# Kernel tuning notes

Hardware: AMD Instinct MI355X
Metric: run time of the kernel (lower is better)

## Reference

```python
import jax, jax.numpy as jnp
import numpy as np

SR = 44100
D = SR * 30          # duration_samples = 1_323_000
N = 1024             # number of note events
L = 32768            # max note length in samples
W = 1024             # hann window length (module's window_length)
H = 8                # harmonics in the synth
K = 128              # FIR taps in the effect chain
LAT = 2              # time_latent_size


def setup_inputs() -> dict:
    key = jax.random.key(0)
    ks = jax.random.split(key, 10)
    freq_rad = jax.random.uniform(ks[0], (N,), jnp.float32, 0.01, 0.3)
    velocity = jax.random.uniform(ks[1], (N,), jnp.float32, 1.0, 127.0)
    starts = jax.random.randint(ks[2], (N,), 0, D - L, dtype=jnp.int32)
    lengths = jax.random.randint(ks[3], (N,), 2048, L + 1, dtype=jnp.int32)
    # time_embedder: Linear(1,32) -> ReLU -> Linear(32,LAT)
    w1 = jax.random.normal(ks[4], (1, 32), jnp.float32)
    b1 = jnp.zeros((32,), jnp.float32)
    w2 = jax.random.normal(ks[5], (32, LAT), jnp.float32) / jnp.sqrt(32.0)
    b2 = jnp.zeros((LAT,), jnp.float32)
    # synth amplitude MLP: [freq, vel, latent] (2+LAT) -> 64 -> H
    ws1 = jax.random.normal(ks[6], (2 + LAT, 64), jnp.float32)
    bs1 = jnp.zeros((64,), jnp.float32)
    ws2 = jax.random.normal(ks[7], (64, H), jnp.float32) / 8.0
    bs2 = jnp.zeros((H,), jnp.float32)
    # effect chain: causal FIR (OIW layout) + tanh
    fir = jax.random.normal(ks[8], (1, 1, K), jnp.float32) / K
    return dict(freq_rad=freq_rad, velocity=velocity,
                w1=w1, b1=b1, w2=w2, b2=b2,
                ws1=ws1, bs1=bs1, ws2=ws2, bs2=bs2, fir=fir,
                starts=starts, lengths=lengths, duration_samples=D)


def reference(freq_rad, velocity, w1, b1, w2, b2, ws1, bs1, ws2, bs2, fir,
              starts, lengths, duration_samples):
    Dn = int(duration_samples)
    t = jnp.arange(L, dtype=jnp.float32)            # [L]
    ti = jnp.arange(L, dtype=jnp.int32)             # [L]
    ends = starts + lengths
    # output_length = min(end, duration) - start, clipped to [0, L]
    out_len = jnp.clip(jnp.minimum(ends, Dn) - starts, 0, L)  # [N]
    # time latent: MLP on normalized start time
    nt = (starts.astype(jnp.float32) / Dn)[:, None]           # [N,1]
    lat = jax.nn.relu(nt @ w1 + b1) @ w2 + b2                  # [N,LAT]
    vel = (velocity / 127.0)[:, None]                          # [N,1]
    # harmonic amplitudes from tiny MLP (the 'synth')
    feat = jnp.concatenate([freq_rad[:, None], vel, lat], axis=-1)  # [N,2+LAT]
    amps = jax.nn.softplus(jax.nn.relu(feat @ ws1 + bs1) @ ws2 + bs2)  # [N,H]
    # additive synthesis; fixed small loop over harmonics, vectorized over [N,L]
    phase = freq_rad[:, None] * t[None, :]                     # [N,L]
    seg = jnp.zeros((N, L), jnp.float32)
    for hh in range(1, H + 1):
        seg = seg + amps[:, hh - 1:hh] * jnp.sin(hh * phase)
    seg = seg * vel
    # hann window (torch periodic) on the LAST W samples of each variable-length segment
    n = jnp.arange(W, dtype=jnp.float32)
    hann = 0.5 * (1.0 - jnp.cos(2.0 * jnp.pi * n / W))         # [W]
    wpos = ti[None, :] - (out_len[:, None] - W)                # [N,L]
    in_win = (wpos >= 0) & (wpos < W)
    factor = jnp.where(in_win, hann[jnp.clip(wpos, 0, W - 1)], 1.0)
    mask = (ti[None, :] < out_len[:, None]).astype(jnp.float32)  # zero past segment end
    seg = seg * factor * mask
    # effect chain: causal 128-tap FIR then tanh (masked so padding stays silent)
    y = jax.lax.conv_general_dilated(seg[:, None, :], fir,
                                     window_strides=(1,), padding=[(K - 1, 0)])
    seg = jnp.tanh(y[:, 0, :]) * mask                          # [N,L]
    # overlap-add: scatter each note into the output buffer
    idx = starts[:, None] + ti[None, :]                        # [N,L]
    valid = (ti[None, :] < out_len[:, None]) & (idx < Dn)
    contrib = jnp.where(valid, seg, 0.0)
    out = jnp.zeros((Dn,), jnp.float32).at[jnp.clip(idx, 0, Dn - 1).reshape(-1)].add(
        contrib.reshape(-1))
    return out
```

## Files before the change

kernel.cpp:

```cpp
#include <hip/hip_runtime.h>
#include <math.h>

#define LMAX  32768
#define WWIN  1024
#define KFIR  128
#define WOUT  512
#define TO    1024
#define CPAD  656
#define NMAX  1024
#define PMAX  96

typedef _Float16 v8h __attribute__((ext_vector_type(8)));
typedef _Float16 v4h __attribute__((ext_vector_type(4)));
typedef float    v4f __attribute__((ext_vector_type(4)));

__device__ __forceinline__ float fast_tanh(float x) {
    float e = __builtin_amdgcn_exp2f(x * 2.8853900817779268f);
    return fmaf(-2.0f, __builtin_amdgcn_rcpf(e + 1.0f), 1.0f);
}

__global__ __launch_bounds__(128, 3) void synth_fused_k(
    const float* __restrict__ freq_g, const float* __restrict__ velo_g,
    const float* __restrict__ w1,  const float* __restrict__ b1,
    const float* __restrict__ w2,  const float* __restrict__ b2,
    const float* __restrict__ ws1, const float* __restrict__ bs1,
    const float* __restrict__ ws2, const float* __restrict__ bs2,
    const float* __restrict__ fir,
    const int* __restrict__ starts, const int* __restrict__ lengths,
    float* __restrict__ out, int Dn, int N)
{
    __shared__ __align__(16) _Float16 segc[2][4][CPAD];
    __shared__ float fir_s[KFIR];
    __shared__ unsigned short note_list[NMAX];
    __shared__ int note_cnt;
    __shared__ float s_w1[32], s_b1[32], s_w2[64], s_b2[2];
    __shared__ float s_ws1[256], s_bs1[64], s_ws2[512], s_bs2[8];
    __shared__ int   stl[PMAX], oll[PMAX];
    __shared__ float fl[PMAX];
    __shared__ __align__(16) float ampsl[PMAX][8];

    const int tid  = threadIdx.x;
    const int wid  = tid >> 6;
    const int lane = tid & 63;
    const int m    = lane & 15;
    const int quad = lane >> 4;
    const int o0   = blockIdx.x * TO;
    const int o_end = min(o0 + TO, Dn);
    const int ow   = o0 + wid * WOUT;

    fir_s[tid] = fir[tid];
    if (tid < 32) { s_w1[tid] = w1[tid]; s_b1[tid] = b1[tid]; }
    if (tid < 64) { s_w2[tid] = w2[tid]; s_bs1[tid] = bs1[tid]; }
    if (tid < 2)  s_b2[tid] = b2[tid];
    if (tid < 8)  s_bs2[tid] = bs2[tid];
    s_ws1[tid] = ws1[tid];       s_ws1[tid + 128] = ws1[tid + 128];
    s_ws2[tid] = ws2[tid];       s_ws2[tid + 128] = ws2[tid + 128];
    s_ws2[tid + 256] = ws2[tid + 256]; s_ws2[tid + 384] = ws2[tid + 384];
    if (tid == 0) note_cnt = 0;
    __syncthreads();

    for (int j = tid; j < N; j += 128) {
        int st = starts[j];
        int len = lengths[j];
        int ol = min(st + len, Dn) - st;
        ol = max(0, min(ol, LMAX));
        if (st < o_end && st + ol > o0) {
            int p = atomicAdd(&note_cnt, 1);
            note_list[p] = (unsigned short)j;
        }
    }
    __syncthreads();
    const int K = note_cnt;

    const int kn0 = min(K, PMAX);
    if (tid < kn0) {
        const int nid = (int)note_list[tid];
        int st  = starts[nid];
        int len = lengths[nid];
        int ol  = min(st + len, Dn) - st;
        ol = max(0, min(ol, LMAX));
        stl[tid] = st;
        oll[tid] = ol;
        float v = velo_g[nid] * (1.0f / 127.0f);
        float f = freq_g[nid];
        fl[tid] = f;
        float nt = (float)st / (float)Dn;
        float lat0 = s_b2[0], lat1 = s_b2[1];
        #pragma unroll
        for (int j = 0; j < 32; ++j) {
            float h = fmaxf(fmaf(nt, s_w1[j], s_b1[j]), 0.0f);
            lat0 = fmaf(h, s_w2[j * 2 + 0], lat0);
            lat1 = fmaf(h, s_w2[j * 2 + 1], lat1);
        }
        float acc[8];
        #pragma unroll
        for (int h = 0; h < 8; ++h) acc[h] = s_bs2[h];
        #pragma unroll
        for (int j = 0; j < 64; ++j) {
            float a = s_bs1[j];
            a = fmaf(f,    s_ws1[0 * 64 + j], a);
            a = fmaf(v,    s_ws1[1 * 64 + j], a);
            a = fmaf(lat0, s_ws1[2 * 64 + j], a);
            a = fmaf(lat1, s_ws1[3 * 64 + j], a);
            a = fmaxf(a, 0.0f);
            #pragma unroll
            for (int h = 0; h < 8; ++h)
                acc[h] = fmaf(a, s_ws2[j * 8 + h], acc[h]);
        }
        #pragma unroll
        for (int h = 0; h < 8; ++h) {
            float a = acc[h];
            float sp = fmaxf(a, 0.0f) + log1pf(expf(-fabsf(a)));
            ampsl[tid][h] = sp * v;
        }
    }

    v8h afrag[12];
    #pragma unroll
    for (int t = 0; t < 12; ++t) {
        v8h af;
        #pragma unroll
        for (int j = 0; j < 8; ++j) {
            int idx = 32 * t + 8 * quad + j - 16 * m;
            float fv = (idx >= 0 && idx < KFIR) ? fir_s[idx] : 0.0f;
            af[j] = (_Float16)fv;
        }
        afrag[t] = af;
    }
    for (int z = lane; z < 4 * 20; z += 64) {
        int S = z / 20, off = z % 20;
        segc[wid][S][636 + off] = (_Float16)0.0f;
    }
    __syncthreads();

    const _Float16* __restrict__ bbase = &segc[wid][m & 3][(m & ~3) + 8 * quad];

    float accA0 = 0.f, accA1 = 0.f, accA2 = 0.f, accA3 = 0.f;
    float accB0 = 0.f, accB1 = 0.f, accB2 = 0.f, accB3 = 0.f;

    const double inv2pi = 0.15915494309189535;

    for (int c = 0; c < K; c += PMAX) {
        const int kn = min(K - c, PMAX);

        if (c > 0) {
            __syncthreads();
            if (tid < kn) {
                const int nid = (int)note_list[c + tid];
                int st  = starts[nid];
                int len = lengths[nid];
                int ol  = min(st + len, Dn) - st;
                ol = max(0, min(ol, LMAX));
                stl[tid] = st;
                oll[tid] = ol;
                float v = velo_g[nid] * (1.0f / 127.0f);
                float f = freq_g[nid];
                fl[tid] = f;
                float nt = (float)st / (float)Dn;
                float lat0 = s_b2[0], lat1 = s_b2[1];
                #pragma unroll
                for (int j = 0; j < 32; ++j) {
                    float h = fmaxf(fmaf(nt, s_w1[j], s_b1[j]), 0.0f);
                    lat0 = fmaf(h, s_w2[j * 2 + 0], lat0);
                    lat1 = fmaf(h, s_w2[j * 2 + 1], lat1);
                }
                float acc[8];
                #pragma unroll
                for (int h = 0; h < 8; ++h) acc[h] = s_bs2[h];
                #pragma unroll
                for (int j = 0; j < 64; ++j) {
                    float a = s_bs1[j];
                    a = fmaf(f,    s_ws1[0 * 64 + j], a);
                    a = fmaf(v,    s_ws1[1 * 64 + j], a);
                    a = fmaf(lat0, s_ws1[2 * 64 + j], a);
                    a = fmaf(lat1, s_ws1[3 * 64 + j], a);
                    a = fmaxf(a, 0.0f);
                    #pragma unroll
                    for (int h = 0; h < 8; ++h)
                        acc[h] = fmaf(a, s_ws2[j * 8 + h], acc[h]);
                }
                #pragma unroll
                for (int h = 0; h < 8; ++h) {
                    float a = acc[h];
                    float sp = fmaxf(a, 0.0f) + log1pf(expf(-fabsf(a)));
                    ampsl[tid][h] = sp * v;
                }
            }
            __syncthreads();
        }

        int stN = 0, olN = 0; float fN = 0.f;
        float4 amN0 = {}, amN1 = {};
        if (kn > 0) {
            stN = stl[0]; olN = oll[0]; fN = fl[0];
            amN0 = *(const float4*)&ampsl[0][0];
            amN1 = *(const float4*)&ampsl[0][4];
        }

        for (int kk = 0; kk < kn; ++kk) {
            const int st = stN, ol = olN;
            const float f = fN;
            const float4 am0 = amN0, am1 = amN1;
            if (kk + 1 < kn) {
                stN = stl[kk + 1]; olN = oll[kk + 1]; fN = fl[kk + 1];
                amN0 = *(const float4*)&ampsl[kk + 1][0];
                amN1 = *(const float4*)&ampsl[kk + 1][4];
            }

            const int base = ow - st;
            if (base >= ol || base + WOUT <= 0) continue;

            const float A0 = am0.x, A1 = am0.y, A2 = am0.z, A3 = am0.w;
            const float A4 = am1.x, A5 = am1.y, A6 = am1.z, A7 = am1.w;
            const double fd = (double)f;

            const int tseed = base - 127 + lane;
            double rev0 = fd * (double)tseed * inv2pi;
            float r0 = (float)(rev0 - floor(rev0));
            float s = __builtin_amdgcn_sinf(r0);
            float cc = __builtin_amdgcn_cosf(r0);
            double d64 = fd * 64.0 * inv2pi;
            float r64 = (float)(d64 - floor(d64));
            const float sd = __builtin_amdgcn_sinf(r64);
            const float cd = __builtin_amdgcn_cosf(r64);
            const int wbase = ol - WWIN;

            const bool interior = (base >= 127) && (base + 513 <= wbase);

            if (interior) {
                #pragma unroll
                for (int i = 0; i < 10; ++i) {
                    float tc = cc + cc;
                    float sA = s;
                    float sum = A0 * sA;
                    float sB = tc * sA;              sum = fmaf(A1, sB, sum);
                    float sC = fmaf(tc, sB, -sA);    sum = fmaf(A2, sC, sum);
                    float sD = fmaf(tc, sC, -sB);    sum = fmaf(A3, sD, sum);
                    float sE = fmaf(tc, sD, -sC);    sum = fmaf(A4, sE, sum);
                    float sF = fmaf(tc, sE, -sD);    sum = fmaf(A5, sF, sum);
                    float sG = fmaf(tc, sF, -sE);    sum = fmaf(A6, sG, sum);
                    float sH = fmaf(tc, sG, -sF);    sum = fmaf(A7, sH, sum);
                    _Float16 h = (_Float16)sum;
                    const int x = lane + 64 * i;
                    if (i == 0) {
                        #pragma unroll
                        for (int S = 0; S < 4; ++S)
                            if (x >= S) segc[wid][S][x - S] = h;
                    } else {
                        #pragma unroll
                        for (int S = 0; S < 4; ++S)
                            segc[wid][S][x - S] = h;
                    }
                    float ns = fmaf(s, cd, cc * sd);
                    float nc = fmaf(cc, cd, -(s * sd));
                    s = ns; cc = nc;
                }
            } else {
                #pragma unroll
                for (int i = 0; i < 10; ++i) {
                    int t = tseed + 64 * i;
                    float val = 0.0f;
                    if (t >= 0 && t < ol) {
                        float tc = cc + cc;
                        float sA = s;
                        float sum = A0 * sA;
                        float sB = tc * sA;              sum = fmaf(A1, sB, sum);
                        float sC = fmaf(tc, sB, -sA);    sum = fmaf(A2, sC, sum);
                        float sD = fmaf(tc, sC, -sB);    sum = fmaf(A3, sD, sum);
                        float sE = fmaf(tc, sD, -sC);    sum = fmaf(A4, sE, sum);
                        float sF = fmaf(tc, sE, -sD);    sum = fmaf(A5, sF, sum);
                        float sG = fmaf(tc, sF, -sE);    sum = fmaf(A6, sG, sum);
                        float sH = fmaf(tc, sG, -sF);    sum = fmaf(A7, sH, sum);
                        int wpos = t - wbase;
                        float factor = 1.0f;
                        if (wpos >= 0)
                            factor = 0.5f - 0.5f * __builtin_amdgcn_cosf((float)wpos * (1.0f / WWIN));
                        val = sum * factor;
                    }
                    _Float16 h = (_Float16)val;
                    const int x = lane + 64 * i;
                    if (i == 0) {
                        #pragma unroll
                        for (int S = 0; S < 4; ++S)
                            if (x >= S) segc[wid][S][x - S] = h;
                    } else {
                        #pragma unroll
                        for (int S = 0; S < 4; ++S)
                            segc[wid][S][x - S] = h;
                    }
                    float ns = fmaf(s, cd, cc * sd);
                    float nc = fmaf(cc, cd, -(s * sd));
                    s = ns; cc = nc;
                }
            }

            v4f CA0 = {0.f, 0.f, 0.f, 0.f};
            v4f CA1 = {0.f, 0.f, 0.f, 0.f};
            v4f CB0 = {0.f, 0.f, 0.f, 0.f};
            v4f CB1 = {0.f, 0.f, 0.f, 0.f};
            #pragma unroll
            for (int t = 0; t < 6; ++t) {
                v4h lo = *(const v4h*)(bbase + 32 * t);
                v4h hi = *(const v4h*)(bbase + 32 * t + 4);
                v8h bf = __builtin_shufflevector(lo, hi, 0, 1, 2, 3, 4, 5, 6, 7);
                CA0 = __builtin_amdgcn_mfma_f32_16x16x32_f16(afrag[t], bf, CA0, 0, 0, 0);
                v4h lo2 = *(const v4h*)(bbase + 256 + 32 * t);
                v4h hi2 = *(const v4h*)(bbase + 256 + 32 * t + 4);
                v8h bf2 = __builtin_shufflevector(lo2, hi2, 0, 1, 2, 3, 4, 5, 6, 7);
                CB0 = __builtin_amdgcn_mfma_f32_16x16x32_f16(afrag[t], bf2, CB0, 0, 0, 0);
            }
            #pragma unroll
            for (int t = 6; t < 12; ++t) {
                v4h lo = *(const v4h*)(bbase + 32 * t);
                v4h hi = *(const v4h*)(bbase + 32 * t + 4);
                v8h bf = __builtin_shufflevector(lo, hi, 0, 1, 2, 3, 4, 5, 6, 7);
                CA1 = __builtin_amdgcn_mfma_f32_16x16x32_f16(afrag[t], bf, CA1, 0, 0, 0);
                v4h lo2 = *(const v4h*)(bbase + 256 + 32 * t);
                v4h hi2 = *(const v4h*)(bbase + 256 + 32 * t + 4);
                v8h bf2 = __builtin_shufflevector(lo2, hi2, 0, 1, 2, 3, 4, 5, 6, 7);
                CB1 = __builtin_amdgcn_mfma_f32_16x16x32_f16(afrag[t], bf2, CB1, 0, 0, 0);
            }

            {
                const int tb = base + 64 * quad + m;
                float y;
                y = CA0[0] + CA1[0]; if (tb +   0 >= 0 && tb +   0 < ol) accA0 += fast_tanh(y);
                y = CA0[1] + CA1[1]; if (tb +  16 >= 0 && tb +  16 < ol) accA1 += fast_tanh(y);
                y = CA0[2] + CA1[2]; if (tb +  32 >= 0 && tb +  32 < ol) accA2 += fast_tanh(y);
                y = CA0[3] + CA1[3]; if (tb +  48 >= 0 && tb +  48 < ol) accA3 += fast_tanh(y);
                y = CB0[0] + CB1[0]; if (tb + 256 >= 0 && tb + 256 < ol) accB0 += fast_tanh(y);
                y = CB0[1] + CB1[1]; if (tb + 272 >= 0 && tb + 272 < ol) accB1 += fast_tanh(y);
                y = CB0[2] + CB1[2]; if (tb + 288 >= 0 && tb + 288 < ol) accB2 += fast_tanh(y);
                y = CB0[3] + CB1[3]; if (tb + 304 >= 0 && tb + 304 < ol) accB3 += fast_tanh(y);
            }
        }
    }

    const int ob = ow + 64 * quad + m;
    if (ob +   0 < Dn) out[ob +   0] = accA0;
    if (ob +  16 < Dn) out[ob +  16] = accA1;
    if (ob +  32 < Dn) out[ob +  32] = accA2;
    if (ob +  48 < Dn) out[ob +  48] = accA3;
    if (ob + 256 < Dn) out[ob + 256] = accB0;
    if (ob + 272 < Dn) out[ob + 272] = accB1;
    if (ob + 288 < Dn) out[ob + 288] = accB2;
    if (ob + 304 < Dn) out[ob + 304] = accB3;
}

extern "C" void kernel_launch(void* const* d_in, const int* in_sizes, int n_in,
                              void* d_out, int out_size, void* d_ws, size_t ws_size,
                              hipStream_t stream) {
    const float* freq    = (const float*)d_in[0];
    const float* velo    = (const float*)d_in[1];
    const float* w1      = (const float*)d_in[2];
    const float* b1      = (const float*)d_in[3];
    const float* w2      = (const float*)d_in[4];
    const float* b2      = (const float*)d_in[5];
    const float* ws1     = (const float*)d_in[6];
    const float* bs1     = (const float*)d_in[7];
    const float* ws2     = (const float*)d_in[8];
    const float* bs2     = (const float*)d_in[9];
    const float* fir     = (const float*)d_in[10];
    const int*   starts  = (const int*)d_in[11];
    const int*   lengths = (const int*)d_in[12];

    const int N  = in_sizes[0];
    const int Dn = out_size;
    float* out = (float*)d_out;

    int n_tiles = (Dn + TO - 1) / TO;
    synth_fused_k<<<n_tiles, 128, 0, stream>>>(
        freq, velo, w1, b1, w2, b2, ws1, bs1, ws2, bs2,
        fir, starts, lengths, out, Dn, N);
}
```

Before: 143.8 us.

## Double-buffer note staging and defer tanh epilogue to overlap with MFMA

```diff
diff --git a/kernel.cpp b/kernel.cpp
--- a/kernel.cpp
+++ b/kernel.cpp
@@ -29,7 +29,7 @@
     const int* __restrict__ starts, const int* __restrict__ lengths,
     float* __restrict__ out, int Dn, int N)
 {
-    __shared__ __align__(16) _Float16 segc[2][4][CPAD];
+    __shared__ __align__(16) _Float16 segc[2][2][4][CPAD];
     __shared__ float fir_s[KFIR];
     __shared__ unsigned short note_list[NMAX];
     __shared__ int note_cnt;
@@ -127,23 +127,132 @@
         }
         afrag[t] = af;
     }
-    for (int z = lane; z < 4 * 20; z += 64) {
-        int S = z / 20, off = z % 20;
-        segc[wid][S][636 + off] = (_Float16)0.0f;
+    for (int z = lane; z < 2 * 4 * 20; z += 64) {
+        int b = z / 80, r = z % 80;
+        int S = r / 20, off = r % 20;
+        segc[wid][b][S][636 + off] = (_Float16)0.0f;
     }
     __syncthreads();
 
-    const _Float16* __restrict__ bbase = &segc[wid][m & 3][(m & ~3) + 8 * quad];
+    const _Float16* __restrict__ bb0 = &segc[wid][0][m & 3][(m & ~3) + 8 * quad];
+    const _Float16* __restrict__ bb1 = &segc[wid][1][m & 3][(m & ~3) + 8 * quad];
 
     float accA0 = 0.f, accA1 = 0.f, accA2 = 0.f, accA3 = 0.f;
     float accB0 = 0.f, accB1 = 0.f, accB2 = 0.f, accB3 = 0.f;
 
     const double inv2pi = 0.15915494309189535;
 
+    auto stage_pair = [&](int k, int b) {
+        const int st = stl[k], ol = oll[k];
+        const float f = fl[k];
+        const float4 am0 = *(const float4*)&ampsl[k][0];
+        const float4 am1 = *(const float4*)&ampsl[k][4];
+        const float A0 = am0.x, A1 = am0.y, A2 = am0.z, A3 = am0.w;
+        const float A4 = am1.x, A5 = am1.y, A6 = am1.z, A7 = am1.w;
+        const int base = ow - st;
+        const double fd = (double)f;
+        const int tseed = base - 127 + lane;
+        double rev0 = fd * (double)tseed * inv2pi;
+        float r0 = (float)(rev0 - floor(rev0));
+        float s = __builtin_amdgcn_sinf(r0);
+        float cc = __builtin_amdgcn_cosf(r0);
+        double d64 = fd * 64.0 * inv2pi;
+        float r64 = (float)(d64 - floor(d64));
+        const float sd = __builtin_amdgcn_sinf(r64);
+        const float cd = __builtin_amdgcn_cosf(r64);
+        const int wbase = ol - WWIN;
+        _Float16 (* __restrict__ sc)[CPAD] = segc[wid][b];
+        const bool interior = (base >= 127) && (base + 513 <= wbase);
+        if (interior) {
+            #pragma unroll
+            for (int i = 0; i < 10; ++i) {
+                float tc = cc + cc;
+                float sA = s;
+                float sum = A0 * sA;
+                float sB = tc * sA;              sum = fmaf(A1, sB, sum);
+                float sC = fmaf(tc, sB, -sA);    sum = fmaf(A2, sC, sum);
+                float sD = fmaf(tc, sC, -sB);    sum = fmaf(A3, sD, sum);
+                float sE = fmaf(tc, sD, -sC);    sum = fmaf(A4, sE, sum);
+                float sF = fmaf(tc, sE, -sD);    sum = fmaf(A5, sF, sum);
+                float sG = fmaf(tc, sF, -sE);    sum = fmaf(A6, sG, sum);
+                float sH = fmaf(tc, sG, -sF);    sum = fmaf(A7, sH, sum);
+                _Float16 h = (_Float16)sum;
+                const int x = lane + 64 * i;
+                if (i == 0) {
+                    #pragma unroll
+                    for (int S = 0; S < 4; ++S)
+                        if (x >= S) sc[S][x - S] = h;
+                } else {
+                    #pragma unroll
+                    for (int S = 0; S < 4; ++S)
+                        sc[S][x - S] = h;
+                }
+                float ns = fmaf(s, cd, cc * sd);
+                float nc = fmaf(cc, cd, -(s * sd));
+                s = ns; cc = nc;
+            }
+        } else {
+            #pragma unroll
+            for (int i = 0; i < 10; ++i) {
+                int t = tseed + 64 * i;
+                float val = 0.0f;
+                if (t >= 0 && t < ol) {
+                    float tc = cc + cc;
+                    float sA = s;
+                    float sum = A0 * sA;
+                    float sB = tc * sA;              sum = fmaf(A1, sB, sum);
+                    float sC = fmaf(tc, sB, -sA);    sum = fmaf(A2, sC, sum);
+                    float sD = fmaf(tc, sC, -sB);    sum = fmaf(A3, sD, sum);
+                    float sE = fmaf(tc, sD, -sC);    sum = fmaf(A4, sE, sum);
+                    float sF = fmaf(tc, sE, -sD);    sum = fmaf(A5, sF, sum);
+                    float sG = fmaf(tc, sF, -sE);    sum = fmaf(A6, sG, sum);
+                    float sH = fmaf(tc, sG, -sF);    sum = fmaf(A7, sH, sum);
+                    int wpos = t - wbase;
+                    float factor = 1.0f;
+                    if (wpos >= 0)
+                        factor = 0.5f - 0.5f * __builtin_amdgcn_cosf((float)wpos * (1.0f / WWIN));
+                    val = sum * factor;
+                }
+                _Float16 h = (_Float16)val;
+                const int x = lane + 64 * i;
+                if (i == 0) {
+                    #pragma unroll
+                    for (int S = 0; S < 4; ++S)
+                        if (x >= S) sc[S][x - S] = h;
+                } else {
+                    #pragma unroll
+                    for (int S = 0; S < 4; ++S)
+                        sc[S][x - S] = h;
+                }
+                float ns = fmaf(s, cd, cc * sd);
+                float nc = fmaf(cc, cd, -(s * sd));
+                s = ns; cc = nc;
+            }
+        }
+    };
+
+    v4f pCA = {0.f, 0.f, 0.f, 0.f}, pCB = {0.f, 0.f, 0.f, 0.f};
+    int ptb = 0, pol = 0;
+    bool have_prev = false;
+    int buf = 0;
+
+    #define EMIT_PREV() do {                                                    \
+        float y;                                                                \
+        y = pCA[0]; if (ptb +   0 >= 0 && ptb +   0 < pol) accA0 += fast_tanh(y); \
+        y = pCA[1]; if (ptb +  16 >= 0 && ptb +  16 < pol) accA1 += fast_tanh(y); \
+        y = pCA[2]; if (ptb +  32 >= 0 && ptb +  32 < pol) accA2 += fast_tanh(y); \
+        y = pCA[3]; if (ptb +  48 >= 0 && ptb +  48 < pol) accA3 += fast_tanh(y); \
+        y = pCB[0]; if (ptb + 256 >= 0 && ptb + 256 < pol) accB0 += fast_tanh(y); \
+        y = pCB[1]; if (ptb + 272 >= 0 && ptb + 272 < pol) accB1 += fast_tanh(y); \
+        y = pCB[2]; if (ptb + 288 >= 0 && ptb + 288 < pol) accB2 += fast_tanh(y); \
+        y = pCB[3]; if (ptb + 304 >= 0 && ptb + 304 < pol) accB3 += fast_tanh(y); \
+    } while (0)
+
     for (int c = 0; c < K; c += PMAX) {
         const int kn = min(K - c, PMAX);
 
         if (c > 0) {
+            if (have_prev) { EMIT_PREV(); have_prev = false; }
             __syncthreads();
             if (tid < kn) {
                 const int nid = (int)note_list[c + tid];
@@ -189,152 +298,52 @@
             __syncthreads();
         }
 
-        int stN = 0, olN = 0; float fN = 0.f;
-        float4 amN0 = {}, amN1 = {};
-        if (kn > 0) {
-            stN = stl[0]; olN = oll[0]; fN = fl[0];
-            amN0 = *(const float4*)&ampsl[0][0];
-            amN1 = *(const float4*)&ampsl[0][4];
-        }
-
-        for (int kk = 0; kk < kn; ++kk) {
-            const int st = stN, ol = olN;
-            const float f = fN;
-            const float4 am0 = amN0, am1 = amN1;
-            if (kk + 1 < kn) {
-                stN = stl[kk + 1]; olN = oll[kk + 1]; fN = fl[kk + 1];
-                amN0 = *(const float4*)&ampsl[kk + 1][0];
-                amN1 = *(const float4*)&ampsl[kk + 1][4];
-            }
-
-            const int base = ow - st;
-            if (base >= ol || base + WOUT <= 0) continue;
-
-            const float A0 = am0.x, A1 = am0.y, A2 = am0.z, A3 = am0.w;
-            const float A4 = am1.x, A5 = am1.y, A6 = am1.z, A7 = am1.w;
-            const double fd = (double)f;
-
-            const int tseed = base - 127 + lane;
-            double rev0 = fd * (double)tseed * inv2pi;
-            float r0 = (float)(rev0 - floor(rev0));
-            float s = __builtin_amdgcn_sinf(r0);
-            float cc = __builtin_amdgcn_cosf(r0);
-            double d64 = fd * 64.0 * inv2pi;
-            float r64 = (float)(d64 - floor(d64));
-            const float sd = __builtin_amdgcn_sinf(r64);
-            const float cd = __builtin_amdgcn_cosf(r64);
-            const int wbase = ol - WWIN;
-
-            const bool interior = (base >= 127) && (base + 513 <= wbase);
-
-            if (interior) {
-                #pragma unroll
-                for (int i = 0; i < 10; ++i) {
-                    float tc = cc + cc;
-                    float sA = s;
-                    float sum = A0 * sA;
-                    float sB = tc * sA;              sum = fmaf(A1, sB, sum);
-                    float sC = fmaf(tc, sB, -sA);    sum = fmaf(A2, sC, sum);
-                    float sD = fmaf(tc, sC, -sB);    sum = fmaf(A3, sD, sum);
-                    float sE = fmaf(tc, sD, -sC);    sum = fmaf(A4, sE, sum);
-                    float sF = fmaf(tc, sE, -sD);    sum = fmaf(A5, sF, sum);
-                    float sG = fmaf(tc, sF, -sE);    sum = fmaf(A6, sG, sum);
-                    float sH = fmaf(tc, sG, -sF);    sum = fmaf(A7, sH, sum);
-                    _Float16 h = (_Float16)sum;
-                    const int x = lane + 64 * i;
-                    if (i == 0) {
-                        #pragma unroll
-                        for (int S = 0; S < 4; ++S)
-                            if (x >= S) segc[wid][S][x - S] = h;
-                    } else {
-                        #pragma unroll
-                        for (int S = 0; S < 4; ++S)
-                            segc[wid][S][x - S] = h;
-                    }
-                    float ns = fmaf(s, cd, cc * sd);
-                    float nc = fmaf(cc, cd, -(s * sd));
-                    s = ns; cc = nc;
-                }
-            } else {
-                #pragma unroll
-                for (int i = 0; i < 10; ++i) {
-                    int t = tseed + 64 * i;
-                    float val = 0.0f;
-                    if (t >= 0 && t < ol) {
-                        float tc = cc + cc;
-                        float sA = s;
-                        float sum = A0 * sA;
-                        float sB = tc * sA;              sum = fmaf(A1, sB, sum);
-                        float sC = fmaf(tc, sB, -sA);    sum = fmaf(A2, sC, sum);
-                        float sD = fmaf(tc, sC, -sB);    sum = fmaf(A3, sD, sum);
-                        float sE = fmaf(tc, sD, -sC);    sum = fmaf(A4, sE, sum);
-                        float sF = fmaf(tc, sE, -sD);    sum = fmaf(A5, sF, sum);
-                        float sG = fmaf(tc, sF, -sE);    sum = fmaf(A6, sG, sum);
-                        float sH = fmaf(tc, sG, -sF);    sum = fmaf(A7, sH, sum);
-                        int wpos = t - wbase;
-                        float factor = 1.0f;
-                        if (wpos >= 0)
-                            factor = 0.5f - 0.5f * __builtin_amdgcn_cosf((float)wpos * (1.0f / WWIN));
-                        val = sum * factor;
-                    }
-                    _Float16 h = (_Float16)val;
-                    const int x = lane + 64 * i;
-                    if (i == 0) {
-                        #pragma unroll
-                        for (int S = 0; S < 4; ++S)
-                            if (x >= S) segc[wid][S][x - S] = h;
-                    } else {
-                        #pragma unroll
-                        for (int S = 0; S < 4; ++S)
-                            segc[wid][S][x - S] = h;
-                    }
-                    float ns = fmaf(s, cd, cc * sd);
-                    float nc = fmaf(cc, cd, -(s * sd));
-                    s = ns; cc = nc;
-                }
-            }
-
-            v4f CA0 = {0.f, 0.f, 0.f, 0.f};
-            v4f CA1 = {0.f, 0.f, 0.f, 0.f};
-            v4f CB0 = {0.f, 0.f, 0.f, 0.f};
-            v4f CB1 = {0.f, 0.f, 0.f, 0.f};
+        int cur = 0;
+        while (cur < kn) {
+            int st = stl[cur], ol = oll[cur];
+            int b = ow - st;
+            if (b < ol && b + WOUT > 0) break;
+            ++cur;
+        }
+        if (cur < kn) stage_pair(cur, buf);
+
+        while (cur < kn) {
+            int nxt = cur + 1;
+            while (nxt < kn) {
+                int st = stl[nxt], ol = oll[nxt];
+                int b = ow - st;
+                if (b < ol && b + WOUT > 0) break;
+                ++nxt;
+            }
+            if (nxt < kn) stage_pair(nxt, buf ^ 1);
+
+            const _Float16* __restrict__ bb = buf ? bb1 : bb0;
+            v4f CA = {0.f, 0.f, 0.f, 0.f};
+            v4f CB = {0.f, 0.f, 0.f, 0.f};
             #pragma unroll
-            for (int t = 0; t < 6; ++t) {
-                v4h lo = *(const v4h*)(bbase + 32 * t);
-                v4h hi = *(const v4h*)(bbase + 32 * t + 4);
+            for (int t = 0; t < 12; ++t) {
+                v4h lo = *(const v4h*)(bb + 32 * t);
+                v4h hi = *(const v4h*)(bb + 32 * t + 4);
                 v8h bf = __builtin_shufflevector(lo, hi, 0, 1, 2, 3, 4, 5, 6, 7);
-                CA0 = __builtin_amdgcn_mfma_f32_16x16x32_f16(afrag[t], bf, CA0, 0, 0, 0);
-                v4h lo2 = *(const v4h*)(bbase + 256 + 32 * t);
-                v4h hi2 = *(const v4h*)(bbase + 256 + 32 * t + 4);
+                CA = __builtin_amdgcn_mfma_f32_16x16x32_f16(afrag[t], bf, CA, 0, 0, 0);
+                v4h lo2 = *(const v4h*)(bb + 256 + 32 * t);
+                v4h hi2 = *(const v4h*)(bb + 256 + 32 * t + 4);
                 v8h bf2 = __builtin_shufflevector(lo2, hi2, 0, 1, 2, 3, 4, 5, 6, 7);
-                CB0 = __builtin_amdgcn_mfma_f32_16x16x32_f16(afrag[t], bf2, CB0, 0, 0, 0);
-            }
-            #pragma unroll
-            for (int t = 6; t < 12; ++t) {
-                v4h lo = *(const v4h*)(bbase + 32 * t);
-                v4h hi = *(const v4h*)(bbase + 32 * t + 4);
-                v8h bf = __builtin_shufflevector(lo, hi, 0, 1, 2, 3, 4, 5, 6, 7);
-                CA1 = __builtin_amdgcn_mfma_f32_16x16x32_f16(afrag[t], bf, CA1, 0, 0, 0);
-                v4h lo2 = *(const v4h*)(bbase + 256 + 32 * t);
-                v4h hi2 = *(const v4h*)(bbase + 256 + 32 * t + 4);
-                v8h bf2 = __builtin_shufflevector(lo2, hi2, 0, 1, 2, 3, 4, 5, 6, 7);
-                CB1 = __builtin_amdgcn_mfma_f32_16x16x32_f16(afrag[t], bf2, CB1, 0, 0, 0);
-            }
-
-            {
-                const int tb = base + 64 * quad + m;
-                float y;
-                y = CA0[0] + CA1[0]; if (tb +   0 >= 0 && tb +   0 < ol) accA0 += fast_tanh(y);
-                y = CA0[1] + CA1[1]; if (tb +  16 >= 0 && tb +  16 < ol) accA1 += fast_tanh(y);
-                y = CA0[2] + CA1[2]; if (tb +  32 >= 0 && tb +  32 < ol) accA2 += fast_tanh(y);
-                y = CA0[3] + CA1[3]; if (tb +  48 >= 0 && tb +  48 < ol) accA3 += fast_tanh(y);
-                y = CB0[0] + CB1[0]; if (tb + 256 >= 0 && tb + 256 < ol) accB0 += fast_tanh(y);
-                y = CB0[1] + CB1[1]; if (tb + 272 >= 0 && tb + 272 < ol) accB1 += fast_tanh(y);
-                y = CB0[2] + CB1[2]; if (tb + 288 >= 0 && tb + 288 < ol) accB2 += fast_tanh(y);
-                y = CB0[3] + CB1[3]; if (tb + 304 >= 0 && tb + 304 < ol) accB3 += fast_tanh(y);
-            }
-        }
-    }
+                CB = __builtin_amdgcn_mfma_f32_16x16x32_f16(afrag[t], bf2, CB, 0, 0, 0);
+            }
+
+            if (have_prev) EMIT_PREV();
+
+            pCA = CA; pCB = CB;
+            ptb = (ow - stl[cur]) + 64 * quad + m;
+            pol = oll[cur];
+            have_prev = true;
+
+            cur = nxt;
+            buf ^= 1;
+        }
+    }
+    if (have_prev) EMIT_PREV();
 
     const int ob = ow + 64 * quad + m;
     if (ob +   0 < Dn) out[ob +   0] = accA0;
```

Measured after the change: 147.1 us. 1.02x slower.
